# Kernel optimization log

Hardware: AMD Instinct MI355X
Metric: run time of the kernel (lower is better)

Reference implementation:

```python
import jax, jax.numpy as jnp
import numpy as np

VOCAB = 32000
HID = 512
T_IN = 128
T_OUT = 128
BATCH = 32


def gru_scan(xs, h0, W, U, bi, br):
    """Keras GRUCell (reset_after=True) over time.
    xs: [T, B, H] inputs; h0: [B, H]; W: [H, 3H]; U: [H, 3H]; bi, br: [3H].
    Returns (h_final [B,H], hs [T,B,H])."""
    # input projections for all timesteps at once
    x_proj = jnp.einsum('tbh,hg->tbg', xs, W) + bi  # [T, B, 3H]

    def step(h, xp):
        rec = h @ U + br                      # [B, 3H]
        xz, xr, xh = jnp.split(xp, 3, axis=-1)
        rz, rr, rh = jnp.split(rec, 3, axis=-1)
        z = jax.nn.sigmoid(xz + rz)
        r = jax.nn.sigmoid(xr + rr)
        hh = jnp.tanh(xh + r * rh)
        h_new = z * h + (1.0 - z) * hh
        return h_new, h_new

    h_final, hs = jax.lax.scan(step, h0, x_proj)
    return h_final, hs


def setup_inputs() -> dict:
    key = jax.random.key(0)
    ks = jax.random.split(key, 12)
    s = 0.05
    return {
        'inputs': jax.random.randint(ks[0], (BATCH, T_IN), 0, VOCAB, dtype=jnp.int64 if jax.config.jax_enable_x64 else jnp.int32),
        'emb': jax.random.normal(ks[1], (VOCAB, HID), jnp.float32) * s,
        'enc_W': jax.random.normal(ks[2], (HID, 3 * HID), jnp.float32) * s,
        'enc_U': jax.random.normal(ks[3], (HID, 3 * HID), jnp.float32) * s,
        'enc_bi': jnp.zeros((3 * HID,), jnp.float32),
        'enc_br': jnp.zeros((3 * HID,), jnp.float32),
        'dec_W': jax.random.normal(ks[4], (HID, 3 * HID), jnp.float32) * s,
        'dec_U': jax.random.normal(ks[5], (HID, 3 * HID), jnp.float32) * s,
        'dec_bi': jnp.zeros((3 * HID,), jnp.float32),
        'dec_br': jnp.zeros((3 * HID,), jnp.float32),
        'w_relu': jax.random.normal(ks[6], (HID, HID), jnp.float32) * s,
        'b_relu': jnp.zeros((HID,), jnp.float32),
        'w_out': jax.random.normal(ks[7], (HID, VOCAB), jnp.float32) * s,
        'b_out': jnp.zeros((VOCAB,), jnp.float32),
    }


def reference(inputs, emb, enc_W, enc_U, enc_bi, enc_br,
              dec_W, dec_U, dec_bi, dec_br, w_relu, b_relu, w_out, b_out):
    B = inputs.shape[0]
    # Embedding lookup: [B, T_in, H] -> time-major [T_in, B, H]
    x = jnp.transpose(emb[inputs], (1, 0, 2))
    h0 = jnp.zeros((B, HID), jnp.float32)
    # Encoder GRU -> final state
    h_enc, _ = gru_scan(x, h0, enc_W, enc_U, enc_bi, enc_br)
    # RepeatVector: decoder input is encoder state at every target step
    dec_in = jnp.broadcast_to(h_enc[None], (T_OUT, B, HID))
    # Decoder GRU with fresh zero state, return sequences
    _, hs = gru_scan(dec_in, h0, dec_W, dec_U, dec_bi, dec_br)  # [T_out, B, H]
    hs = jnp.transpose(hs, (1, 0, 2))  # [B, T_out, H]
    # TimeDistributed Dense+relu, then Dense+softmax over vocab
    h1 = jax.nn.relu(jnp.einsum('bth,hk->btk', hs, w_relu) + b_relu)
    logits = jnp.einsum('bth,hv->btv', h1, w_out) + b_out
    return jax.nn.softmax(logits, axis=-1)
```

## Files before the change

kernel.cpp:

```cpp
#include <hip/hip_runtime.h>
#include <stdint.h>

#define VOCAB 32000
#define HID   512
#define G3    1536
#define TT    128
#define BB    32
#define NROW  4096
#define NCB   250

typedef __attribute__((ext_vector_type(8))) short short8;
typedef __attribute__((ext_vector_type(4))) short short4v;
typedef __attribute__((ext_vector_type(4))) float f32x4;
typedef __attribute__((ext_vector_type(2))) unsigned long long u64x2;

__device__ __forceinline__ unsigned short f2bf(float f) {
  unsigned int u = __builtin_bit_cast(unsigned int, f);
  u += 0x7fffu + ((u >> 16) & 1u);
  return (unsigned short)(u >> 16);
}

__device__ __forceinline__ void gload16(const void* g, void* l) {
  __builtin_amdgcn_global_load_lds(
      (const __attribute__((address_space(1))) unsigned int*)g,
      (__attribute__((address_space(3))) unsigned int*)l, 16, 0, 0);
}

__global__ void convert_bf16_k(const float* __restrict__ src,
                               unsigned short* __restrict__ dst, int n) {
  int i = (blockIdx.x * blockDim.x + threadIdx.x) * 8;
  int stride = gridDim.x * blockDim.x * 8;
  for (; i < n; i += stride) {
    float4 a = *(const float4*)(src + i);
    float4 b = *(const float4*)(src + i + 4);
    short8 o;
    o[0] = (short)f2bf(a.x); o[1] = (short)f2bf(a.y);
    o[2] = (short)f2bf(a.z); o[3] = (short)f2bf(a.w);
    o[4] = (short)f2bf(b.x); o[5] = (short)f2bf(b.y);
    o[6] = (short)f2bf(b.z); o[7] = (short)f2bf(b.w);
    *(short8*)(dst + i) = o;
  }
}

__global__ void transpose_bf16_k(const float* __restrict__ src,
                                 unsigned short* __restrict__ dst,
                                 int K, int N) {
  __shared__ float t[64][65];
  int k0 = blockIdx.x * 64, n0 = blockIdx.y * 64;
  int c = threadIdx.x & 15, rr = threadIdx.x >> 4;
#pragma unroll
  for (int i = 0; i < 4; ++i) {
    float4 v = *(const float4*)(src + (size_t)(k0 + rr + 16 * i) * N + n0 + c * 4);
    t[rr + 16 * i][c * 4 + 0] = v.x;
    t[rr + 16 * i][c * 4 + 1] = v.y;
    t[rr + 16 * i][c * 4 + 2] = v.z;
    t[rr + 16 * i][c * 4 + 3] = v.w;
  }
  __syncthreads();
#pragma unroll
  for (int i = 0; i < 4; ++i) {
    short4v o;
#pragma unroll
    for (int j = 0; j < 4; ++j) o[j] = (short)f2bf(t[c * 4 + j][rr + 16 * i]);
    *(short4v*)(dst + (size_t)(n0 + rr + 16 * i) * K + k0 + c * 4) = o;
  }
}

__global__ void embed_k(const int* __restrict__ inputs,
                        const float* __restrict__ emb,
                        unsigned short* __restrict__ xb) {
  int r = blockIdx.x;
  int t = r >> 5, b = r & 31;
  int idx = inputs[b * TT + t];
  const float* src = emb + (size_t)idx * HID;
  unsigned short* dst = xb + (size_t)r * HID;
  int j = threadIdx.x * 4;
  float4 v = *(const float4*)(src + j);
  short4v o;
  o[0] = (short)f2bf(v.x); o[1] = (short)f2bf(v.y);
  o[2] = (short)f2bf(v.z); o[3] = (short)f2bf(v.w);
  *(short4v*)(dst + j) = o;
}

template<int MODE>
__launch_bounds__(256)
__global__ void gemm_bt(const unsigned short* __restrict__ A,
                        const unsigned short* __restrict__ BT,
                        const float* __restrict__ bias,
                        void* __restrict__ Cv,
                        float* __restrict__ partials,
                        int M, int N, int K) {
  __shared__ unsigned short As[8192];
  __shared__ unsigned short Bs[8192];
  __shared__ float rsum[2][128];
  int tid = threadIdx.x;
  int l = tid & 63;
  int w = tid >> 6;
  int wm = w >> 1, wn = w & 1;
  int row0 = blockIdx.x * 128;
  int col0 = blockIdx.y * 128;

  int sr = (w << 5) + (l >> 3);
  int sg = ((l & 7) ^ ((l >> 3) & 7)) << 3;
  const unsigned short* Ag = A  + (size_t)(row0 + sr) * K + sg;
  const unsigned short* Bg = BT + (size_t)(col0 + sr) * K + sg;

  int cA = l & 15, q = l >> 4, x7 = l & 7;
  const char* asp = (const char*)As;
  const char* bsp = (const char*)Bs;

  f32x4 acc[4][4];
#pragma unroll
  for (int m = 0; m < 4; ++m)
#pragma unroll
    for (int n = 0; n < 4; ++n) acc[m][n] = (f32x4){0.f, 0.f, 0.f, 0.f};

  for (int k0 = 0; k0 < K; k0 += 64) {
    if (k0) __syncthreads();
#pragma unroll
    for (int i = 0; i < 4; ++i) {
      gload16(Ag + (size_t)(i * 8) * K + k0, As + ((w << 2) + i) * 512);
      gload16(Bg + (size_t)(i * 8) * K + k0, Bs + ((w << 2) + i) * 512);
    }
    __syncthreads();
#pragma unroll
    for (int kk = 0; kk < 2; ++kk) {
      int sl = (((kk << 2) + q) ^ x7) << 4;
      short8 af[4], bf[4];
#pragma unroll
      for (int m = 0; m < 4; ++m)
        af[m] = *(const short8*)(asp + (wm * 64 + m * 16 + cA) * 128 + sl);
#pragma unroll
      for (int n = 0; n < 4; ++n)
        bf[n] = *(const short8*)(bsp + (wn * 64 + n * 16 + cA) * 128 + sl);
#pragma unroll
      for (int m = 0; m < 4; ++m)
#pragma unroll
        for (int n = 0; n < 4; ++n)
          acc[m][n] = __builtin_amdgcn_mfma_f32_16x16x32_bf16(af[m], bf[n],
                                                              acc[m][n], 0, 0, 0);
    }
  }

  if (MODE == 0 || MODE == 1) {
#pragma unroll
    for (int m = 0; m < 4; ++m)
#pragma unroll
      for (int n = 0; n < 4; ++n) {
        int col = col0 + wn * 64 + n * 16 + cA;
        float bv = bias[col];
#pragma unroll
        for (int r = 0; r < 4; ++r) {
          int row = row0 + wm * 64 + m * 16 + q * 4 + r;
          float v = acc[m][n][r] + bv;
          if (MODE == 0)
            ((float*)Cv)[(size_t)row * N + col] = v;
          else
            ((unsigned short*)Cv)[(size_t)row * N + col] = f2bf(fmaxf(v, 0.f));
        }
      }
  } else {
    float ps[4][4];
#pragma unroll
    for (int m = 0; m < 4; ++m)
#pragma unroll
      for (int r = 0; r < 4; ++r) ps[m][r] = 0.f;
#pragma unroll
    for (int m = 0; m < 4; ++m)
#pragma unroll
      for (int n = 0; n < 4; ++n) {
        int col = col0 + wn * 64 + n * 16 + cA;
        float bv = bias[col];
#pragma unroll
        for (int r = 0; r < 4; ++r) {
          int row = row0 + wm * 64 + m * 16 + q * 4 + r;
          float v = __expf(acc[m][n][r] + bv);
          ((float*)Cv)[(size_t)row * N + col] = v;
          ps[m][r] += v;
        }
      }
#pragma unroll
    for (int mask = 1; mask < 16; mask <<= 1)
#pragma unroll
      for (int m = 0; m < 4; ++m)
#pragma unroll
        for (int r = 0; r < 4; ++r)
          ps[m][r] += __shfl_xor(ps[m][r], mask, 64);
    if (cA == 0) {
#pragma unroll
      for (int m = 0; m < 4; ++m)
#pragma unroll
        for (int r = 0; r < 4; ++r)
          rsum[wn][wm * 64 + m * 16 + q * 4 + r] = ps[m][r];
    }
    __syncthreads();
    if (tid < 128)
      partials[(size_t)blockIdx.y * NROW + row0 + tid] =
          rsum[0][tid] + rsum[1][tid];
  }
}

__launch_bounds__(256)
__global__ void gemm_small_k(const unsigned short* __restrict__ A,
                             const unsigned short* __restrict__ B,
                             const float* __restrict__ bias,
                             float* __restrict__ C,
                             int M, int N, int K) {
  __shared__ unsigned short As[64][56];
  __shared__ unsigned short Bs[64][56];
  int tid = threadIdx.x;
  int lane = tid & 63;
  int w = tid >> 6;
  int wm = w >> 1, wn = w & 1;
  int row0 = blockIdx.x * 64;
  int n0 = blockIdx.y * 64;

  f32x4 acc[2][2];
#pragma unroll
  for (int a = 0; a < 2; ++a)
#pragma unroll
    for (int c = 0; c < 2; ++c) acc[a][c] = (f32x4){0.f, 0.f, 0.f, 0.f};

  for (int k0 = 0; k0 < K; k0 += 32) {
    {
      int row = tid >> 2;
      int kg = (tid & 3) * 8;
      short8 v = {};
      if (row0 + row < M)
        v = *(const short8*)(A + (size_t)(row0 + row) * K + k0 + kg);
      *(short8*)&As[row][kg] = v;
    }
    {
      int k = tid >> 3;
      int ng = (tid & 7) * 8;
      short8 v = *(const short8*)(B + (size_t)(k0 + k) * N + n0 + ng);
#pragma unroll
      for (int qq = 0; qq < 8; ++qq) Bs[ng + qq][k] = (unsigned short)v[qq];
    }
    __syncthreads();
    int kb = (lane >> 4) * 8;
    short8 af0 = *(const short8*)&As[wm * 32 + (lane & 15)][kb];
    short8 af1 = *(const short8*)&As[wm * 32 + 16 + (lane & 15)][kb];
    short8 bf0 = *(const short8*)&Bs[wn * 32 + (lane & 15)][kb];
    short8 bf1 = *(const short8*)&Bs[wn * 32 + 16 + (lane & 15)][kb];
    acc[0][0] = __builtin_amdgcn_mfma_f32_16x16x32_bf16(af0, bf0, acc[0][0], 0, 0, 0);
    acc[0][1] = __builtin_amdgcn_mfma_f32_16x16x32_bf16(af0, bf1, acc[0][1], 0, 0, 0);
    acc[1][0] = __builtin_amdgcn_mfma_f32_16x16x32_bf16(af1, bf0, acc[1][0], 0, 0, 0);
    acc[1][1] = __builtin_amdgcn_mfma_f32_16x16x32_bf16(af1, bf1, acc[1][1], 0, 0, 0);
    __syncthreads();
  }
#pragma unroll
  for (int tm = 0; tm < 2; ++tm)
#pragma unroll
    for (int tn = 0; tn < 2; ++tn) {
      int col = n0 + wn * 32 + tn * 16 + (lane & 15);
      float bv = bias[col];
#pragma unroll
      for (int r = 0; r < 4; ++r) {
        int row = row0 + wm * 32 + tm * 16 + ((lane >> 4) * 4) + r;
        if (row < M)
          C[(size_t)row * N + col] = acc[tm][tn][r] + bv;
      }
    }
}

template<int XPT, int WRITE_ALL>
__launch_bounds__(512)
__global__ void gru_k(const float* __restrict__ U,
                      const float* __restrict__ xp,
                      const float* __restrict__ br,
                      unsigned short* __restrict__ hpub,
                      unsigned short* __restrict__ hsout,
                      unsigned int* __restrict__ flags) {
  __shared__ unsigned short ub[16 * 3 * 64 * 8];
  __shared__ unsigned short hbuf[16384];
  __shared__ float recbuf[3][32][16];
  int tid = threadIdx.x;
  int lane = tid & 63;
  int w = tid >> 6;
  int g = blockIdx.x;
  char* hbase = (char*)hbuf;

  for (int idx = tid; idx < 16 * 3 * 64 * 8; idx += 512) {
    int i = idx & 7;
    int l = (idx >> 3) & 63;
    int rem = idx >> 9;
    int nt = rem % 3;
    int ks = rem / 3;
    int k = ks * 32 + ((l >> 4) * 8) + i;
    int col = nt * 512 + g * 16 + (l & 15);
    ub[idx] = f2bf(U[(size_t)k * G3 + col]);
  }
  int b = tid >> 4, j = tid & 15;
  float br_z = br[g * 16 + j];
  float br_r = br[512 + g * 16 + j];
  float br_h = br[1024 + g * 16 + j];
  float hreg = 0.f;
  __syncthreads();

  int mt = w / 3, nt = w % 3;
  for (int t = 0; t < TT; ++t) {
    size_t xbase = ((size_t)(t * XPT + b)) * G3 + g * 16 + j;
    float xz = xp[xbase], xr = xp[xbase + 512], xh = xp[xbase + 1024];

    float rz, rr, rh;
    if (t == 0) {
      rz = 0.f; rr = 0.f; rh = 0.f;
    } else {
      {
        const unsigned long long* hr =
            (const unsigned long long*)(hpub + ((t & 1) ? 16384 : 0));
        int r = tid >> 4, s = tid & 15;
        unsigned long long av[8];
#pragma unroll
        for (int k = 0; k < 4; ++k) {
          const unsigned long long* p = hr + (size_t)r * 128 + (s + 16 * k) * 2;
          av[2 * k]     = __hip_atomic_load(p,     __ATOMIC_RELAXED,
                                            __HIP_MEMORY_SCOPE_AGENT);
          av[2 * k + 1] = __hip_atomic_load(p + 1, __ATOMIC_RELAXED,
                                            __HIP_MEMORY_SCOPE_AGENT);
        }
        int rx = (r & 7) << 4;
#pragma unroll
        for (int k = 0; k < 4; ++k) {
          int wb = (r * 1024 + (s + 16 * k) * 16) ^ rx;
          u64x2 v;
          v[0] = av[2 * k];
          v[1] = av[2 * k + 1];
          *(u64x2*)(hbase + wb) = v;
        }
      }
      __syncthreads();

      if (w < 6) {
        int arow = mt * 16 + (lane & 15);
        int rx = (arow & 7) << 4;
        int abase = arow * 1024 + (lane >> 4) * 16;
        f32x4 acc = (f32x4){0.f, 0.f, 0.f, 0.f};
#pragma unroll
        for (int ks = 0; ks < 16; ++ks) {
          short8 af = *(const short8*)(hbase + ((abase + ks * 64) ^ rx));
          short8 bf = *(const short8*)&ub[((ks * 3 + nt) * 64 + lane) * 8];
          acc = __builtin_amdgcn_mfma_f32_16x16x32_bf16(af, bf, acc, 0, 0, 0);
        }
#pragma unroll
        for (int r = 0; r < 4; ++r)
          recbuf[nt][mt * 16 + (lane >> 4) * 4 + r][lane & 15] = acc[r];
      }
      __syncthreads();
      rz = recbuf[0][b][j];
      rr = recbuf[1][b][j];
      rh = recbuf[2][b][j];
    }

    float z = 1.f / (1.f + __expf(-(xz + rz + br_z)));
    float rg = 1.f / (1.f + __expf(-(xr + rr + br_r)));
    float pre = xh + rg * (rh + br_h);
    pre = fminf(fmaxf(pre, -15.f), 15.f);
    float e2 = __expf(2.f * pre);
    float hh = (e2 - 1.f) / (e2 + 1.f);
    hreg = z * hreg + (1.f - z) * hh;
    unsigned short hb = f2bf(hreg);
    if (WRITE_ALL)
      hsout[((size_t)b * TT + t) * HID + g * 16 + j] = hb;

    unsigned int hv = (unsigned int)hb;
    unsigned int p1 = (unsigned int)__shfl_xor((int)hv, 1, 64);
    unsigned long long lo = (unsigned long long)((hv & 0xffffu) | (p1 << 16));
    unsigned long long hi = (unsigned long long)__shfl_xor((int)(unsigned int)lo, 2, 64);
    if ((j & 3) == 0) {
      unsigned long long pk = (lo & 0xffffffffull) | (hi << 32);
      unsigned long long* dst = (unsigned long long*)(hpub +
          (((t + 1) & 1) ? 16384 : 0) + b * HID + g * 16 + j);
      __hip_atomic_store(dst, pk, __ATOMIC_RELAXED, __HIP_MEMORY_SCOPE_AGENT);
    }

    if (t + 1 < TT) {
      asm volatile("s_waitcnt vmcnt(0)" ::: "memory");
      __syncthreads();
      if (tid == 0)
        __hip_atomic_store(flags + g * 32, (unsigned)(t + 1),
                           __ATOMIC_RELAXED, __HIP_MEMORY_SCOPE_AGENT);
      if (w == 0 && lane < 32) {
        const unsigned int* fp = flags + lane * 32;
        while (__hip_atomic_load(fp, __ATOMIC_RELAXED,
                                 __HIP_MEMORY_SCOPE_AGENT) < (unsigned)(t + 1)) {}
      }
      __syncthreads();
    }
  }
}

__global__ void rowsum_k(const float* __restrict__ part, float* __restrict__ inv) {
  int r = blockIdx.x * blockDim.x + threadIdx.x;
  float s = 0.f;
  for (int c = 0; c < NCB; ++c) s += part[(size_t)c * NROW + r];
  inv[r] = 1.f / s;
}

__global__ void norm_k(float* __restrict__ out, const float* __restrict__ inv) {
  const unsigned int total4 = (unsigned int)NROW * (VOCAB / 4);
  unsigned int stride = gridDim.x * blockDim.x;
  for (unsigned int i = blockIdx.x * blockDim.x + threadIdx.x; i < total4;
       i += stride) {
    unsigned int row = i / (VOCAB / 4);
    float s = inv[row];
    float4* p = (float4*)out + i;
    float4 v = *p;
    v.x *= s; v.y *= s; v.z *= s; v.w *= s;
    *p = v;
  }
}

extern "C" void kernel_launch(void* const* d_in, const int* in_sizes, int n_in,
                              void* d_out, int out_size, void* d_ws, size_t ws_size,
                              hipStream_t stream) {
  const int*   inputs = (const int*)d_in[0];
  const float* emb    = (const float*)d_in[1];
  const float* encW   = (const float*)d_in[2];
  const float* encU   = (const float*)d_in[3];
  const float* enc_bi = (const float*)d_in[4];
  const float* enc_br = (const float*)d_in[5];
  const float* decW   = (const float*)d_in[6];
  const float* decU   = (const float*)d_in[7];
  const float* dec_bi = (const float*)d_in[8];
  const float* dec_br = (const float*)d_in[9];
  const float* w_relu = (const float*)d_in[10];
  const float* b_relu = (const float*)d_in[11];
  const float* w_out  = (const float*)d_in[12];
  const float* b_out  = (const float*)d_in[13];

  char* ws = (char*)d_ws;
  const size_t o_xproj  = 0;
  const size_t o_xb     = 25165824;
  const size_t o_encWbT = 29360128;
  const size_t o_decWb  = 30932992;
  const size_t o_wrelubT= 32505856;
  const size_t o_woutbT = 33030144;
  const size_t o_decxp  = 65798144;
  const size_t o_hsb    = 65994752;
  const size_t o_h1b    = 70189056;
  const size_t o_part   = 74383360;
  const size_t o_inv    = 82575360;
  const size_t o_hpubE  = 82591744;
  const size_t o_hpubD  = 82657280;

  float*          xproj   = (float*)(ws + o_xproj);
  unsigned short* xb      = (unsigned short*)(ws + o_xb);
  unsigned short* encWbT  = (unsigned short*)(ws + o_encWbT);
  unsigned short* decWb   = (unsigned short*)(ws + o_decWb);
  unsigned short* wrelubT = (unsigned short*)(ws + o_wrelubT);
  unsigned short* woutbT  = (unsigned short*)(ws + o_woutbT);
  float*          decxp   = (float*)(ws + o_decxp);
  unsigned short* hsb     = (unsigned short*)(ws + o_hsb);
  unsigned short* h1b     = (unsigned short*)(ws + o_h1b);
  float*          part    = (float*)(ws + o_part);
  float*          inv     = (float*)(ws + o_inv);
  unsigned short* hpubE   = (unsigned short*)(ws + o_hpubE);
  unsigned short* hpubD   = (unsigned short*)(ws + o_hpubD);
  unsigned int*   flagsE  = (unsigned int*)(ws + o_part);
  unsigned int*   flagsD  = (unsigned int*)(ws + o_part + 4096);

  (void)hipMemsetAsync(ws + o_part, 0, 8192, stream);

  transpose_bf16_k<<<dim3(8, 24), 256, 0, stream>>>(encW, encWbT, HID, G3);
  transpose_bf16_k<<<dim3(8, 8), 256, 0, stream>>>(w_relu, wrelubT, HID, HID);
  transpose_bf16_k<<<dim3(8, 500), 256, 0, stream>>>(w_out, woutbT, HID, VOCAB);
  convert_bf16_k<<<384, 256, 0, stream>>>(decW, decWb, 512 * G3);

  embed_k<<<4096, 128, 0, stream>>>(inputs, emb, xb);

  gemm_bt<0><<<dim3(32, 12), 256, 0, stream>>>(xb, encWbT, enc_bi, xproj,
                                               nullptr, NROW, G3, HID);
  gru_k<32, 0><<<32, 512, 0, stream>>>(encU, xproj, enc_br, hpubE, nullptr, flagsE);

  gemm_small_k<<<dim3(1, 24), 256, 0, stream>>>(hpubE, decWb, dec_bi, decxp,
                                                BB, G3, HID);
  gru_k<0, 1><<<32, 512, 0, stream>>>(decU, decxp, dec_br, hpubD, hsb, flagsD);

  gemm_bt<1><<<dim3(32, 4), 256, 0, stream>>>(hsb, wrelubT, b_relu, h1b,
                                              nullptr, NROW, HID, HID);
  gemm_bt<2><<<dim3(32, NCB), 256, 0, stream>>>(h1b, woutbT, b_out, d_out, part,
                                                NROW, VOCAB, HID);
  rowsum_k<<<16, 256, 0, stream>>>(part, inv);
  norm_k<<<2048, 256, 0, stream>>>((float*)d_out, inv);
}
```

Measured before the change: 1.436 ms.

## Replace per-step flag barrier with timestamp-tagged hidden-state words in GRU

The GRU kernels used a grid-wide flag barrier each timestep: every block stored its h slice, waited for its stores to drain, synced, published a flag, and polled all 32 flags. Now each 64-bit published word carries two bf16 hidden values plus the step number in its upper half, and readers spin on exactly the words they need until the tag matches. This drops two __syncthreads, the vmcnt drain and the flag polling from the critical path of each recurrent step. In exchange it doubles the published buffer size and adds per-word polling, and it needs a separate final-state buffer because the published layout now holds tags.

```diff
diff --git a/kernel.cpp b/kernel.cpp
--- a/kernel.cpp
+++ b/kernel.cpp
@@ -269,9 +269,8 @@
 __global__ void gru_k(const float* __restrict__ U,
                       const float* __restrict__ xp,
                       const float* __restrict__ br,
-                      unsigned short* __restrict__ hpub,
-                      unsigned short* __restrict__ hsout,
-                      unsigned int* __restrict__ flags) {
+                      unsigned long long* __restrict__ hpub,
+                      unsigned short* __restrict__ hsout) {
   __shared__ unsigned short ub[16 * 3 * 64 * 8];
   __shared__ unsigned short hbuf[16384];
   __shared__ float recbuf[3][32][16];
@@ -308,26 +307,34 @@
       rz = 0.f; rr = 0.f; rh = 0.f;
     } else {
       {
-        const unsigned long long* hr =
-            (const unsigned long long*)(hpub + ((t & 1) ? 16384 : 0));
-        int r = tid >> 4, s = tid & 15;
-        unsigned long long av[8];
-#pragma unroll
-        for (int k = 0; k < 4; ++k) {
-          const unsigned long long* p = hr + (size_t)r * 128 + (s + 16 * k) * 2;
-          av[2 * k]     = __hip_atomic_load(p,     __ATOMIC_RELAXED,
-                                            __HIP_MEMORY_SCOPE_AGENT);
-          av[2 * k + 1] = __hip_atomic_load(p + 1, __ATOMIC_RELAXED,
-                                            __HIP_MEMORY_SCOPE_AGENT);
+        const unsigned long long* src = hpub + (size_t)(t & 1) * 8192 +
+                                        b * 256 + j * 16;
+        unsigned long long v[16];
+#pragma unroll
+        for (int k = 0; k < 16; ++k)
+          v[k] = __hip_atomic_load(src + k, __ATOMIC_RELAXED,
+                                   __HIP_MEMORY_SCOPE_AGENT);
+        unsigned want = (unsigned)t;
+        while (true) {
+          bool ok = true;
+#pragma unroll
+          for (int k = 0; k < 16; ++k)
+            ok = ok && ((unsigned)(v[k] >> 32) == want);
+          if (ok) break;
+#pragma unroll
+          for (int k = 0; k < 16; ++k)
+            if ((unsigned)(v[k] >> 32) != want)
+              v[k] = __hip_atomic_load(src + k, __ATOMIC_RELAXED,
+                                       __HIP_MEMORY_SCOPE_AGENT);
         }
-        int rx = (r & 7) << 4;
-#pragma unroll
-        for (int k = 0; k < 4; ++k) {
-          int wb = (r * 1024 + (s + 16 * k) * 16) ^ rx;
-          u64x2 v;
-          v[0] = av[2 * k];
-          v[1] = av[2 * k + 1];
-          *(u64x2*)(hbase + wb) = v;
+        int rx = (b & 7) << 4;
+#pragma unroll
+        for (int i = 0; i < 4; ++i) {
+          u64x2 pk;
+          pk[0] = (v[4 * i] & 0xffffffffull)     | (v[4 * i + 1] << 32);
+          pk[1] = (v[4 * i + 2] & 0xffffffffull) | (v[4 * i + 3] << 32);
+          int wb = (b * 1024 + (j * 4 + i) * 16) ^ rx;
+          *(u64x2*)(hbase + wb) = pk;
         }
       }
       __syncthreads();
@@ -363,30 +370,17 @@
     unsigned short hb = f2bf(hreg);
     if (WRITE_ALL)
       hsout[((size_t)b * TT + t) * HID + g * 16 + j] = hb;
+    else if (t == TT - 1)
+      hsout[b * HID + g * 16 + j] = hb;
 
     unsigned int hv = (unsigned int)hb;
     unsigned int p1 = (unsigned int)__shfl_xor((int)hv, 1, 64);
-    unsigned long long lo = (unsigned long long)((hv & 0xffffu) | (p1 << 16));
-    unsigned long long hi = (unsigned long long)__shfl_xor((int)(unsigned int)lo, 2, 64);
-    if ((j & 3) == 0) {
-      unsigned long long pk = (lo & 0xffffffffull) | (hi << 32);
-      unsigned long long* dst = (unsigned long long*)(hpub +
-          (((t + 1) & 1) ? 16384 : 0) + b * HID + g * 16 + j);
-      __hip_atomic_store(dst, pk, __ATOMIC_RELAXED, __HIP_MEMORY_SCOPE_AGENT);
-    }
-
-    if (t + 1 < TT) {
-      asm volatile("s_waitcnt vmcnt(0)" ::: "memory");
-      __syncthreads();
-      if (tid == 0)
-        __hip_atomic_store(flags + g * 32, (unsigned)(t + 1),
-                           __ATOMIC_RELAXED, __HIP_MEMORY_SCOPE_AGENT);
-      if (w == 0 && lane < 32) {
-        const unsigned int* fp = flags + lane * 32;
-        while (__hip_atomic_load(fp, __ATOMIC_RELAXED,
-                                 __HIP_MEMORY_SCOPE_AGENT) < (unsigned)(t + 1)) {}
-      }
-      __syncthreads();
+    if ((j & 1) == 0) {
+      unsigned long long val = (unsigned long long)((hv & 0xffffu) | (p1 << 16))
+                             | ((unsigned long long)(unsigned)(t + 1) << 32);
+      unsigned long long* dst = hpub + (size_t)((t + 1) & 1) * 8192 +
+                                b * 256 + g * 8 + (j >> 1);
+      __hip_atomic_store(dst, val, __ATOMIC_RELAXED, __HIP_MEMORY_SCOPE_AGENT);
     }
   }
 }
@@ -443,7 +437,8 @@
   const size_t o_part   = 74383360;
   const size_t o_inv    = 82575360;
   const size_t o_hpubE  = 82591744;
-  const size_t o_hpubD  = 82657280;
+  const size_t o_hpubD  = 82722816;
+  const size_t o_hfinal = 82853888;
 
   float*          xproj   = (float*)(ws + o_xproj);
   unsigned short* xb      = (unsigned short*)(ws + o_xb);
@@ -456,12 +451,11 @@
   unsigned short* h1b     = (unsigned short*)(ws + o_h1b);
   float*          part    = (float*)(ws + o_part);
   float*          inv     = (float*)(ws + o_inv);
-  unsigned short* hpubE   = (unsigned short*)(ws + o_hpubE);
-  unsigned short* hpubD   = (unsigned short*)(ws + o_hpubD);
-  unsigned int*   flagsE  = (unsigned int*)(ws + o_part);
-  unsigned int*   flagsD  = (unsigned int*)(ws + o_part + 4096);
-
-  (void)hipMemsetAsync(ws + o_part, 0, 8192, stream);
+  unsigned long long* hpubE = (unsigned long long*)(ws + o_hpubE);
+  unsigned long long* hpubD = (unsigned long long*)(ws + o_hpubD);
+  unsigned short* hfinal  = (unsigned short*)(ws + o_hfinal);
+
+  (void)hipMemsetAsync(ws + o_hpubE, 0, 131072 * 2, stream);
 
   transpose_bf16_k<<<dim3(8, 24), 256, 0, stream>>>(encW, encWbT, HID, G3);
   transpose_bf16_k<<<dim3(8, 8), 256, 0, stream>>>(w_relu, wrelubT, HID, HID);
@@ -472,11 +466,11 @@
 
   gemm_bt<0><<<dim3(32, 12), 256, 0, stream>>>(xb, encWbT, enc_bi, xproj,
                                                nullptr, NROW, G3, HID);
-  gru_k<32, 0><<<32, 512, 0, stream>>>(encU, xproj, enc_br, hpubE, nullptr, flagsE);
-
-  gemm_small_k<<<dim3(1, 24), 256, 0, stream>>>(hpubE, decWb, dec_bi, decxp,
+  gru_k<32, 0><<<32, 512, 0, stream>>>(encU, xproj, enc_br, hpubE, hfinal);
+
+  gemm_small_k<<<dim3(1, 24), 256, 0, stream>>>(hfinal, decWb, dec_bi, decxp,
                                                 BB, G3, HID);
-  gru_k<0, 1><<<32, 512, 0, stream>>>(decU, decxp, dec_br, hpubD, hsb, flagsD);
+  gru_k<0, 1><<<32, 512, 0, stream>>>(decU, decxp, dec_br, hpubD, hsb);
 
   gemm_bt<1><<<dim3(32, 4), 256, 0, stream>>>(hsb, wrelubT, b_relu, h1b,
                                               nullptr, NROW, HID, HID);
```

Result: slower. 2.595 ms (+80.8%).
